# Performance work log

Hardware: AMD Instinct MI355X
Metric: run time of the kernel (lower is better)

The kernel has to match this reference:

```python
import jax, jax.numpy as jnp
import numpy as np

EPS = 1e-8
LEAK = 0.2


def upsample_linear_2x(x):
    # PyTorch nn.Upsample(scale_factor=2, mode='linear', align_corners=False) on [B,C,L]
    B, C, L = x.shape
    Lo = 2 * L
    coords = jnp.maximum((jnp.arange(Lo, dtype=jnp.float32) + 0.5) / 2.0 - 0.5, 0.0)
    i0 = jnp.minimum(jnp.floor(coords).astype(jnp.int32), L - 1)
    i1 = jnp.minimum(i0 + 1, L - 1)
    w = (coords - i0.astype(jnp.float32)).astype(x.dtype)
    return x[..., i0] * (1.0 - w) + x[..., i1] * w


def mod_conv1d(x, style, W, demod=True):
    # Style-modulated conv (StyleGAN2 Conv2DMod adapted to 1D).
    # x: [B,C,L], style: [B,C], W: [F,C,K]. Equivalent to per-sample weight
    # W*(style+1) (optionally demodulated) via input scaling + shared conv.
    s = style + 1.0
    pad = (W.shape[-1] - 1) // 2
    y = jax.lax.conv_general_dilated(x * s[:, :, None], W, (1,), [(pad, pad)],
                                     dimension_numbers=('NCH', 'OIH', 'NCH'))
    if demod:
        wmod = W[None] * s[:, None, :, None]              # [B,F,C,K]
        d = jax.lax.rsqrt(jnp.sum(wmod * wmod, axis=(2, 3)) + EPS)  # [B,F]
        y = y * d[:, :, None]
    return y


def setup_inputs() -> dict:
    key = jax.random.key(0)
    ks = jax.random.split(key, 12)
    B, Cin, F, L, Z = 8, 256, 128, 2048, 256
    Lu = 2 * L
    inp = {}
    inp['x'] = jax.random.normal(ks[0], (B, Cin, L), jnp.float32)
    inp['prev_rgb'] = jax.random.normal(ks[1], (B, 1, Lu), jnp.float32)
    inp['istyle'] = jax.random.normal(ks[2], (B, Z), jnp.float32)
    inp['inoise'] = jax.random.normal(ks[3], (B, 100), jnp.float32)
    # learned parameters
    inp['style1_w'] = jax.random.normal(ks[4], (Cin, Z), jnp.float32) * 0.02
    inp['style1_b'] = jnp.zeros((Cin,), jnp.float32)
    inp['conv1_w'] = jax.random.normal(ks[5], (F, Cin, 3), jnp.float32) * 0.05
    inp['noise_w1'] = jax.random.normal(ks[6], (F * Lu, 100), jnp.float32) * 0.01
    inp['style2_w'] = jax.random.normal(ks[7], (F, Z), jnp.float32) * 0.02
    inp['style2_b'] = jnp.zeros((F,), jnp.float32)
    inp['conv2_w'] = jax.random.normal(ks[8], (F, F, 3), jnp.float32) * 0.05
    inp['noise_w2'] = jax.random.normal(ks[9], (F * Lu, 100), jnp.float32) * 0.01
    inp['rgb_style_w'] = jax.random.normal(ks[10], (F, Z), jnp.float32) * 0.02
    inp['rgb_style_b'] = jnp.zeros((F,), jnp.float32)
    inp['rgb_conv_w'] = jax.random.normal(ks[11], (1, F, 1), jnp.float32) * 0.05
    return inp


def reference(x, prev_rgb, istyle, inoise, style1_w, style1_b, conv1_w, noise_w1,
              style2_w, style2_b, conv2_w, noise_w2, rgb_style_w, rgb_style_b, rgb_conv_w):
    x = upsample_linear_2x(x)                                 # [B,Cin,Lu]
    s1 = istyle @ style1_w.T + style1_b                       # [B,Cin]
    x = mod_conv1d(x, s1, conv1_w, demod=True)                # [B,F,Lu]
    n1 = (inoise @ noise_w1.T).reshape(x.shape)               # noise injection 1
    x = jax.nn.leaky_relu(x + n1, LEAK)
    s2 = istyle @ style2_w.T + style2_b                       # [B,F]
    x = mod_conv1d(x, s2, conv2_w, demod=True)                # [B,F,Lu]
    n2 = (inoise @ noise_w2.T).reshape(x.shape)               # noise injection 2
    x = jax.nn.leaky_relu(x + n2, LEAK)
    srgb = istyle @ rgb_style_w.T + rgb_style_b               # [B,F]
    rgb = jnp.einsum('bcl,fc->bfl', x * (srgb + 1.0)[:, :, None], rgb_conv_w[:, :, 0])
    rgb = rgb + prev_rgb
    rgb = upsample_linear_2x(rgb)                             # [B,1,2*Lu]
    return (x, rgb)
```

## Files before the change

kernel.cpp:

```cpp
#include <hip/hip_runtime.h>
#include <hip/hip_bf16.h>

#define EPS 1e-8f
#define LEAK 0.2f

#define B 8
#define CIN 256
#define F 128
#define L 2048
#define LU 4096
#define Z 256
#define NZ 100
#define S (F * LU)

typedef __attribute__((ext_vector_type(8))) short bf16x8;
typedef __attribute__((ext_vector_type(4))) float f32x4;

__device__ inline unsigned short f2bf(float x) {
    unsigned u = __builtin_bit_cast(unsigned, x);
    u += 0x7fffu + ((u >> 16) & 1u);
    return (unsigned short)(u >> 16);
}
__device__ inline float bf2f(unsigned short h) {
    unsigned u = ((unsigned)h) << 16;
    return __builtin_bit_cast(float, u);
}
__device__ inline unsigned pack2(float a, float b) {
    __hip_bfloat162 h = __float22bfloat162_rn(make_float2(a, b));
    unsigned u;
    __builtin_memcpy(&u, &h, 4);
    return u;
}
__device__ inline bf16x8 cvtfrag(float4 a, float4 b) {
    uint4 u;
    u.x = pack2(a.x, a.y); u.y = pack2(a.z, a.w);
    u.z = pack2(b.x, b.y); u.w = pack2(b.z, b.w);
    return __builtin_bit_cast(bf16x8, u);
}
__device__ inline void gload_lds16(const void* g, void* l) {
    __builtin_amdgcn_global_load_lds((const __attribute__((address_space(1))) void*)g,
                                     (__attribute__((address_space(3))) void*)l, 16, 0, 0);
}

__global__ void k_styles(const float* __restrict__ istyle,
                         const float* __restrict__ s1w, const float* __restrict__ s1b,
                         const float* __restrict__ s2w, const float* __restrict__ s2b,
                         const float* __restrict__ rgbw, const float* __restrict__ rgbb,
                         const float* __restrict__ rgbcw,
                         const float* __restrict__ W1, const float* __restrict__ W2,
                         float* __restrict__ s1, float* __restrict__ s2,
                         float* __restrict__ srgbS,
                         float* __restrict__ d1, float* __restrict__ d2,
                         unsigned short* __restrict__ Wt1, unsigned short* __restrict__ Wt2) {
    int t = threadIdx.x;
    {
        int i = blockIdx.x * 256 + t;
        if (i < 3 * F * CIN) {
            int kk = i / (F * CIN);
            int rem = i - kk * (F * CIN);
            int f = rem >> 8, c = rem & 255;
            Wt1[i] = f2bf(W1[(f * CIN + c) * 3 + kk]);
        }
        if (i < 3 * F * F) {
            int kk = i / (F * F);
            int rem = i - kk * (F * F);
            int f = rem >> 7, c = rem & 127;
            Wt2[i] = f2bf(W2[(f * F + c) * 3 + kk]);
        }
    }
    if (blockIdx.x >= 8) return;
    __shared__ float is[Z];
    __shared__ float sh1[CIN];
    __shared__ float sh2[F];
    int b = blockIdx.x;
    if (t < Z) is[t] = istyle[b * Z + t];
    __syncthreads();
    {
        float acc = 0.f;
        const float* w = s1w + (size_t)t * Z;
        for (int z = 0; z < Z; z += 4) {
            float4 v = *(const float4*)(w + z);
            acc += v.x * is[z] + v.y * is[z + 1] + v.z * is[z + 2] + v.w * is[z + 3];
        }
        float v = acc + s1b[t] + 1.0f;
        sh1[t] = v;
        s1[b * CIN + t] = v;
    }
    if (t < F) {
        float a2 = 0.f, a3 = 0.f;
        const float* w2 = s2w + (size_t)t * Z;
        const float* w3 = rgbw + (size_t)t * Z;
        for (int z = 0; z < Z; z += 4) {
            float4 u2 = *(const float4*)(w2 + z);
            float4 u3 = *(const float4*)(w3 + z);
            a2 += u2.x * is[z] + u2.y * is[z + 1] + u2.z * is[z + 2] + u2.w * is[z + 3];
            a3 += u3.x * is[z] + u3.y * is[z + 1] + u3.z * is[z + 2] + u3.w * is[z + 3];
        }
        float v2 = a2 + s2b[t] + 1.0f;
        sh2[t] = v2;
        s2[b * F + t] = v2;
        srgbS[b * F + t] = (a3 + rgbb[t] + 1.0f) * rgbcw[t];
    }
    __syncthreads();
    if (t < F) {
        float acc = 0.f;
        const float* w = W1 + (size_t)t * CIN * 3;
        for (int c = 0; c < CIN; c += 4) {
            float4 va = *(const float4*)(w + c * 3);
            float4 vb = *(const float4*)(w + c * 3 + 4);
            float4 vc = *(const float4*)(w + c * 3 + 8);
            float s0 = sh1[c], s1v = sh1[c + 1], s2v = sh1[c + 2], s3 = sh1[c + 3];
            acc += s0 * s0 * (va.x * va.x + va.y * va.y + va.z * va.z);
            acc += s1v * s1v * (va.w * va.w + vb.x * vb.x + vb.y * vb.y);
            acc += s2v * s2v * (vb.z * vb.z + vb.w * vb.w + vc.x * vc.x);
            acc += s3 * s3 * (vc.y * vc.y + vc.z * vc.z + vc.w * vc.w);
        }
        d1[b * F + t] = rsqrtf(acc + EPS);
    } else {
        int f = t - F;
        float acc = 0.f;
        const float* w = W2 + (size_t)f * F * 3;
        for (int c = 0; c < F; c += 4) {
            float4 va = *(const float4*)(w + c * 3);
            float4 vb = *(const float4*)(w + c * 3 + 4);
            float4 vc = *(const float4*)(w + c * 3 + 8);
            float s0 = sh2[c], s1v = sh2[c + 1], s2v = sh2[c + 2], s3 = sh2[c + 3];
            acc += s0 * s0 * (va.x * va.x + va.y * va.y + va.z * va.z);
            acc += s1v * s1v * (va.w * va.w + vb.x * vb.x + vb.y * vb.y);
            acc += s2v * s2v * (vb.z * vb.z + vb.w * vb.w + vc.x * vc.x);
            acc += s3 * s3 * (vc.y * vc.y + vc.z * vc.z + vc.w * vc.w);
        }
        d2[b * F + f] = rsqrtf(acc + EPS);
    }
}

__global__ __launch_bounds__(256) void k_prepx(const float* __restrict__ x,
                                               const float* __restrict__ s1,
                                               unsigned short* __restrict__ xt) {
    int b = blockIdx.z, c0 = blockIdx.y * 64, l0 = blockIdx.x * 64;
    int t = threadIdx.x;
    __shared__ float xj[64][37];
    int j0 = (l0 >> 1) - 1;
    for (int idx = t; idx < 64 * 34; idx += 256) {
        int c = idx / 34, jj = idx - c * 34;
        int j = j0 + jj;
        j = j < 0 ? 0 : (j > L - 1 ? L - 1 : j);
        xj[c][jj] = x[((size_t)(b * CIN + c0 + c)) * L + j];
    }
    __syncthreads();
    int c = t & 63;
    int lg = t >> 6;
    float s = s1[b * CIN + c0 + c];
    for (int li = 0; li < 16; ++li) {
        int ll = lg * 16 + li;
        int l = l0 + ll;
        int j = l >> 1;
        int jj = j - j0;
        float v;
        if (l & 1) {
            v = 0.75f * xj[c][jj] + 0.25f * xj[c][jj + 1];
        } else {
            v = (j == 0) ? xj[c][jj] : (0.25f * xj[c][jj - 1] + 0.75f * xj[c][jj]);
        }
        xt[((size_t)(b * LU + l)) * CIN + c0 + c] = f2bf(v * s);
    }
}

__global__ __launch_bounds__(256) void k_conv1(const unsigned short* __restrict__ xt,
                                               const unsigned short* __restrict__ Wt1,
                                               const float* __restrict__ d1,
                                               unsigned short* __restrict__ y1) {
    const int b0 = blockIdx.y * 2;
    const int l0 = blockIdx.x * 64;
    const int nfb = blockIdx.z * 4;
    const int lane = threadIdx.x & 63, wv = threadIdx.x >> 6;
    const int lbase = l0 + wv * 16;
    const int m = lane & 15, ks = lane >> 4;

    f32x4 acc[2][4];
#pragma unroll
    for (int bb = 0; bb < 2; ++bb)
#pragma unroll
        for (int nf = 0; nf < 4; ++nf) acc[bb][nf] = (f32x4)0.f;

    const unsigned short* xb0 = xt + ((size_t)(b0 + 0) * LU) * CIN + ks * 8;
    const unsigned short* xb1 = xt + ((size_t)(b0 + 1) * LU) * CIN + ks * 8;

#pragma unroll 2
    for (int kc = 0; kc < 8; ++kc) {
#pragma unroll
        for (int kk = 0; kk < 3; ++kk) {
            int lA = lbase + m + kk - 1;
            bf16x8 a0 = (bf16x8)0, a1 = (bf16x8)0;
            if (lA >= 0 && lA < LU) {
                a0 = *(const bf16x8*)&xb0[(size_t)lA * CIN + kc * 32];
                a1 = *(const bf16x8*)&xb1[(size_t)lA * CIN + kc * 32];
            }
#pragma unroll
            for (int nf = 0; nf < 4; ++nf) {
                const bf16x8 w =
                    *(const bf16x8*)&Wt1[((kk * F + (nfb + nf) * 16 + m) << 8) + kc * 32 + ks * 8];
                acc[0][nf] = __builtin_amdgcn_mfma_f32_16x16x32_bf16(a0, w, acc[0][nf], 0, 0, 0);
                acc[1][nf] = __builtin_amdgcn_mfma_f32_16x16x32_bf16(a1, w, acc[1][nf], 0, 0, 0);
            }
        }
    }
#pragma unroll
    for (int bb = 0; bb < 2; ++bb) {
        int b = b0 + bb;
#pragma unroll
        for (int nf = 0; nf < 4; ++nf) {
            int f = (nfb + nf) * 16 + m;
            float dm = d1[b * F + f];
#pragma unroll
            for (int q = 0; q < 4; ++q) {
                int l = lbase + ks * 4 + q;
                y1[((size_t)(b * LU + l) << 7) + f] = f2bf(acc[bb][nf][q] * dm);
            }
        }
    }
}

__global__ __launch_bounds__(256) void k_noise1(unsigned short* y1,
                                                const float* __restrict__ nw,
                                                const float* __restrict__ inoise,
                                                const float* __restrict__ s2) {
    __shared__ float lds[2][6400];
    const int t = threadIdx.x;
    const int lane = t & 63, wv = t >> 6;
    const int n = lane & 15, ks = lane >> 4;
    const bool w0 = (t >> 6) == 0;
    const int f0 = (blockIdx.x >> 8) * 32;
    const int l0 = (blockIdx.x & 255) * 16;
    const int r = wv * 16 + n;
    const int fseg = r >> 1, dl = r & 1;
    const int f = f0 + fseg;

    bf16x8 af[4];
#pragma unroll
    for (int ck = 0; ck < 4; ++ck) {
        bf16x8 a = (bf16x8)0;
        if (n < 8) {
            const float* ap = inoise + n * NZ;
#pragma unroll
            for (int j = 0; j < 8; ++j) {
                int z = ck * 32 + ks * 8 + j;
                if (z < NZ) a[j] = (short)f2bf(ap[z]);
            }
        }
        af[ck] = a;
    }

    unsigned short yv[8][4] = {};
    float s2v[4] = {};
    if (ks < 2) {
#pragma unroll
        for (int q = 0; q < 4; ++q) s2v[q] = s2[(ks * 4 + q) * F + f];
#pragma unroll
        for (int cc = 0; cc < 8; ++cc) {
            int l = l0 + 2 * cc + dl;
            size_t i = (size_t)l * F + f;
#pragma unroll
            for (int q = 0; q < 4; ++q) yv[cc][q] = y1[(size_t)(ks * 4 + q) * S + i];
        }
    }

    auto stage = [&](int buf, int cc) {
        const int lbase = l0 + 2 * cc;
#pragma unroll
        for (int rr = 0; rr < 7; ++rr) {
            int g = rr * 256 + t;
            if (g < 1600) {
                int fs = g / 50;
                int rem = g - fs * 50;
                int d2 = (rem >= 25) ? 1 : 0;
                int m = rem - 25 * d2;
                const float* src = nw + ((size_t)(f0 + fs) * LU + lbase + d2) * NZ + m * 4;
                gload_lds16(src, &lds[buf][g * 4]);
            }
        }
    };

    auto compute = [&](int buf, int cc) {
        const float* rowp = &lds[buf][r * 100];
        f32x4 acc = (f32x4)0.f;
#pragma unroll
        for (int ck = 0; ck < 3; ++ck) {
            float4 u0 = *(const float4*)&rowp[ck * 32 + ks * 8];
            float4 u1 = *(const float4*)&rowp[ck * 32 + ks * 8 + 4];
            acc = __builtin_amdgcn_mfma_f32_16x16x32_bf16(af[ck], cvtfrag(u0, u1), acc, 0, 0, 0);
        }
        {
            bf16x8 b3 = (bf16x8)0;
            if (ks == 0) {
                float4 u = *(const float4*)&rowp[96];
                unsigned p0 = pack2(u.x, u.y), p1 = pack2(u.z, u.w);
                b3[0] = (short)(p0 & 0xffff); b3[1] = (short)(p0 >> 16);
                b3[2] = (short)(p1 & 0xffff); b3[3] = (short)(p1 >> 16);
            }
            acc = __builtin_amdgcn_mfma_f32_16x16x32_bf16(af[3], b3, acc, 0, 0, 0);
        }
        if (ks < 2) {
            const int l = l0 + 2 * cc + dl;
            const size_t i = (size_t)l * F + f;
#pragma unroll
            for (int q = 0; q < 4; ++q) {
                float val = bf2f(yv[cc][q]) + acc[q];
                val = val >= 0.f ? val : LEAK * val;
                y1[(size_t)(ks * 4 + q) * S + i] = f2bf(val * s2v[q]);
            }
        }
    };

    stage(0, 0);
    stage(1, 1);

#define WSTEP(N0, N1)                                                       \
    if (w0) { asm volatile("s_waitcnt vmcnt(" #N0 ")" ::: "memory"); }      \
    else    { asm volatile("s_waitcnt vmcnt(" #N1 ")" ::: "memory"); }      \
    __builtin_amdgcn_s_barrier();                                           \
    __builtin_amdgcn_sched_barrier(0);

    WSTEP(7, 6)              compute(0, 0);
    WSTEP(4, 4) stage(0, 2); compute(1, 1);
    WSTEP(4, 4) stage(1, 3); compute(0, 2);
    WSTEP(4, 4) stage(0, 4); compute(1, 3);
    WSTEP(4, 4) stage(1, 5); compute(0, 4);
    WSTEP(4, 4) stage(0, 6); compute(1, 5);
    WSTEP(4, 4) stage(1, 7); compute(0, 6);
    WSTEP(4, 4)              compute(1, 7);
#undef WSTEP
}

__global__ __launch_bounds__(256) void k_conv2(const unsigned short* __restrict__ y1n,
                                               const unsigned short* __restrict__ Wt2,
                                               const float* __restrict__ d2,
                                               float* __restrict__ xout) {
    const int b0 = blockIdx.y * 2;
    const int l0 = blockIdx.x * 64;
    const int mfb = blockIdx.z * 4;
    const int lane = threadIdx.x & 63, wv = threadIdx.x >> 6;
    const int lbase = l0 + wv * 16;
    const int m = lane & 15, ks = lane >> 4;

    f32x4 acc[2][4];
#pragma unroll
    for (int bb = 0; bb < 2; ++bb)
#pragma unroll
        for (int mf = 0; mf < 4; ++mf) acc[bb][mf] = (f32x4)0.f;

    const unsigned short* yb0 = y1n + ((size_t)(b0 + 0) * LU) * F + ks * 8;
    const unsigned short* yb1 = y1n + ((size_t)(b0 + 1) * LU) * F + ks * 8;

#pragma unroll 2
    for (int kc = 0; kc < 4; ++kc) {
#pragma unroll
        for (int kk = 0; kk < 3; ++kk) {
            int lB = lbase + m + kk - 1;
            bf16x8 bv0 = (bf16x8)0, bv1 = (bf16x8)0;
            if (lB >= 0 && lB < LU) {
                bv0 = *(const bf16x8*)&yb0[(size_t)lB * F + kc * 32];
                bv1 = *(const bf16x8*)&yb1[(size_t)lB * F + kc * 32];
            }
#pragma unroll
            for (int mf = 0; mf < 4; ++mf) {
                const bf16x8 w =
                    *(const bf16x8*)&Wt2[((kk * F + (mfb + mf) * 16 + m) << 7) + kc * 32 + ks * 8];
                acc[0][mf] = __builtin_amdgcn_mfma_f32_16x16x32_bf16(w, bv0, acc[0][mf], 0, 0, 0);
                acc[1][mf] = __builtin_amdgcn_mfma_f32_16x16x32_bf16(w, bv1, acc[1][mf], 0, 0, 0);
            }
        }
    }
#pragma unroll
    for (int bb = 0; bb < 2; ++bb) {
        int b = b0 + bb;
#pragma unroll
        for (int mf = 0; mf < 4; ++mf) {
#pragma unroll
            for (int q = 0; q < 4; ++q) {
                int f = (mfb + mf) * 16 + ks * 4 + q;
                int l = lbase + m;
                xout[((size_t)(b * F + f) << 12) + l] = acc[bb][mf][q] * d2[b * F + f];
            }
        }
    }
}

__global__ __launch_bounds__(256) void k_noise2(const float* __restrict__ nw,
                                                const float* __restrict__ inoise,
                                                float* xio) {
    __shared__ float lds[2][6400];
    const int t = threadIdx.x;
    const int lane = t & 63, wv = t >> 6;
    const int n = lane & 15, ks = lane >> 4;
    const bool w0 = (t >> 6) == 0;
    const int row0 = blockIdx.x * 512;
    const int r = wv * 16 + n;

    bf16x8 af[4];
#pragma unroll
    for (int ck = 0; ck < 4; ++ck) {
        bf16x8 a = (bf16x8)0;
        if (n < 8) {
            const float* ap = inoise + n * NZ;
#pragma unroll
            for (int j = 0; j < 8; ++j) {
                int z = ck * 32 + ks * 8 + j;
                if (z < NZ) a[j] = (short)f2bf(ap[z]);
            }
        }
        af[ck] = a;
    }

    float xv[8][4] = {};
    if (ks < 2) {
#pragma unroll
        for (int cc = 0; cc < 8; ++cc) {
            size_t i = (size_t)row0 + cc * 64 + r;
#pragma unroll
            for (int q = 0; q < 4; ++q) xv[cc][q] = xio[(size_t)(ks * 4 + q) * S + i];
        }
    }

    auto stage = [&](int buf, int cc) {
        const float* src0 = nw + ((size_t)row0 + cc * 64) * NZ;
#pragma unroll
        for (int rr = 0; rr < 7; ++rr) {
            int g = rr * 256 + t;
            if (g < 1600) gload_lds16(src0 + g * 4, &lds[buf][g * 4]);
        }
    };

    auto compute = [&](int buf, int cc) {
        const float* rowp = &lds[buf][r * 100];
        f32x4 acc = (f32x4)0.f;
#pragma unroll
        for (int ck = 0; ck < 3; ++ck) {
            float4 u0 = *(const float4*)&rowp[ck * 32 + ks * 8];
            float4 u1 = *(const float4*)&rowp[ck * 32 + ks * 8 + 4];
            acc = __builtin_amdgcn_mfma_f32_16x16x32_bf16(af[ck], cvtfrag(u0, u1), acc, 0, 0, 0);
        }
        {
            bf16x8 b3 = (bf16x8)0;
            if (ks == 0) {
                float4 u = *(const float4*)&rowp[96];
                unsigned p0 = pack2(u.x, u.y), p1 = pack2(u.z, u.w);
                b3[0] = (short)(p0 & 0xffff); b3[1] = (short)(p0 >> 16);
                b3[2] = (short)(p1 & 0xffff); b3[3] = (short)(p1 >> 16);
            }
            acc = __builtin_amdgcn_mfma_f32_16x16x32_bf16(af[3], b3, acc, 0, 0, 0);
        }
        if (ks < 2) {
            const size_t i = (size_t)row0 + cc * 64 + r;
#pragma unroll
            for (int q = 0; q < 4; ++q) {
                float val = xv[cc][q] + acc[q];
                val = val >= 0.f ? val : LEAK * val;
                xio[(size_t)(ks * 4 + q) * S + i] = val;
            }
        }
    };

    stage(0, 0);
    stage(1, 1);

#define WSTEP(N0, N1)                                                       \
    if (w0) { asm volatile("s_waitcnt vmcnt(" #N0 ")" ::: "memory"); }      \
    else    { asm volatile("s_waitcnt vmcnt(" #N1 ")" ::: "memory"); }      \
    __builtin_amdgcn_s_barrier();                                           \
    __builtin_amdgcn_sched_barrier(0);

    WSTEP(7, 6)              compute(0, 0);
    WSTEP(4, 4) stage(0, 2); compute(1, 1);
    WSTEP(4, 4) stage(1, 3); compute(0, 2);
    WSTEP(4, 4) stage(0, 4); compute(1, 3);
    WSTEP(4, 4) stage(1, 5); compute(0, 4);
    WSTEP(4, 4) stage(0, 6); compute(1, 5);
    WSTEP(4, 4) stage(1, 7); compute(0, 6);
    WSTEP(4, 4)              compute(1, 7);
#undef WSTEP
}

__global__ __launch_bounds__(256) void k_rgb(const float* __restrict__ xf,
                                             const float* __restrict__ srgbS,
                                             const float* __restrict__ prev,
                                             float* __restrict__ rgb) {
    int b = blockIdx.y;
    int o0 = blockIdx.x * 512;
    int t = threadIdx.x;
    __shared__ float ss[F];
    __shared__ float pre[258];
    if (t < F) ss[t] = srgbS[b * F + t];
    __syncthreads();
    int j0 = (o0 >> 1) - 1;
    for (int jj = t; jj < 258; jj += 256) {
        int j = j0 + jj;
        j = j < 0 ? 0 : (j > LU - 1 ? LU - 1 : j);
        float acc = prev[b * LU + j];
        const float* xb = xf + (size_t)b * S + j;
        for (int f = 0; f < F; ++f) acc += xb[(size_t)f * LU] * ss[f];
        pre[jj] = acc;
    }
    __syncthreads();
    int jj = t + 1;
    int j = j0 + jj;
    float ve = (j == 0) ? pre[jj] : (0.25f * pre[jj - 1] + 0.75f * pre[jj]);
    float vo = 0.75f * pre[jj] + 0.25f * pre[jj + 1];
    float2 v2 = make_float2(ve, vo);
    *(float2*)&rgb[(size_t)b * 2 * LU + o0 + 2 * t] = v2;
}

extern "C" void kernel_launch(void* const* d_in, const int* in_sizes, int n_in,
                              void* d_out, int out_size, void* d_ws, size_t ws_size,
                              hipStream_t stream) {
    const float* x      = (const float*)d_in[0];
    const float* prev   = (const float*)d_in[1];
    const float* istyle = (const float*)d_in[2];
    const float* inoise = (const float*)d_in[3];
    const float* s1w    = (const float*)d_in[4];
    const float* s1b    = (const float*)d_in[5];
    const float* W1     = (const float*)d_in[6];
    const float* nw1    = (const float*)d_in[7];
    const float* s2w    = (const float*)d_in[8];
    const float* s2b    = (const float*)d_in[9];
    const float* W2     = (const float*)d_in[10];
    const float* nw2    = (const float*)d_in[11];
    const float* rgbw   = (const float*)d_in[12];
    const float* rgbb   = (const float*)d_in[13];
    const float* rgbcw  = (const float*)d_in[14];

    char* w = (char*)d_ws;
    float* s1      = (float*)(w);
    float* s2      = (float*)(w + 8 * 1024);
    float* srgbS   = (float*)(w + 12 * 1024);
    float* d1      = (float*)(w + 16 * 1024);
    float* d2      = (float*)(w + 20 * 1024);
    unsigned short* Wt1 = (unsigned short*)(w + 256 * 1024);
    unsigned short* Wt2 = (unsigned short*)(w + 448 * 1024);
    unsigned short* y1  = (unsigned short*)(w + (size_t)1024 * 1024);

    unsigned short* xt = (unsigned short*)d_out;

    float* xout   = (float*)d_out;
    float* rgbout = xout + (size_t)B * S;

    k_styles<<<384, 256, 0, stream>>>(istyle, s1w, s1b, s2w, s2b, rgbw, rgbb, rgbcw,
                                      W1, W2, s1, s2, srgbS, d1, d2, Wt1, Wt2);
    k_prepx<<<dim3(LU / 64, CIN / 64, B), 256, 0, stream>>>(x, s1, xt);
    k_conv1<<<dim3(LU / 64, B / 2, 2), 256, 0, stream>>>(xt, Wt1, d1, y1);
    k_noise1<<<1024, 256, 0, stream>>>(y1, nw1, inoise, s2);
    k_conv2<<<dim3(LU / 64, B / 2, 2), 256, 0, stream>>>(y1, Wt2, d2, xout);
    k_noise2<<<1024, 256, 0, stream>>>(nw2, inoise, xout);
    k_rgb<<<dim3(2 * LU / 512, B), 256, 0, stream>>>(xout, srgbS, prev, rgbout);
}
```

Measured before the change: 239.5 us.

## Merge conv1 and both noise GEMMs into one launch, apply noise later

Conv1 and the two noise-projection GEMMs now run together in one grid, split by block index, so the memory-bound noise-weight streaming can overlap with the conv1 MFMA work. The noise results go to new bf16 scratch buffers. A small elementwise kernel then adds noise 1, applies leaky-relu and the s2 scale. Noise 2 and its leaky-relu are folded into the conv2 epilogue, which removes the separate read-modify-write pass over the fp32 output. In exchange it writes and reads two extra bf16 intermediates, adds one launch, and rounds noise 2 to bf16 before adding it.

```diff
diff --git a/kernel.cpp b/kernel.cpp
--- a/kernel.cpp
+++ b/kernel.cpp
@@ -166,75 +166,81 @@
     }
 }
 
-__global__ __launch_bounds__(256) void k_conv1(const unsigned short* __restrict__ xt,
-                                               const unsigned short* __restrict__ Wt1,
-                                               const float* __restrict__ d1,
-                                               unsigned short* __restrict__ y1) {
-    const int b0 = blockIdx.y * 2;
-    const int l0 = blockIdx.x * 64;
-    const int nfb = blockIdx.z * 4;
-    const int lane = threadIdx.x & 63, wv = threadIdx.x >> 6;
-    const int lbase = l0 + wv * 16;
-    const int m = lane & 15, ks = lane >> 4;
-
-    f32x4 acc[2][4];
-#pragma unroll
-    for (int bb = 0; bb < 2; ++bb)
-#pragma unroll
-        for (int nf = 0; nf < 4; ++nf) acc[bb][nf] = (f32x4)0.f;
-
-    const unsigned short* xb0 = xt + ((size_t)(b0 + 0) * LU) * CIN + ks * 8;
-    const unsigned short* xb1 = xt + ((size_t)(b0 + 1) * LU) * CIN + ks * 8;
-
-#pragma unroll 2
-    for (int kc = 0; kc < 8; ++kc) {
-#pragma unroll
-        for (int kk = 0; kk < 3; ++kk) {
-            int lA = lbase + m + kk - 1;
-            bf16x8 a0 = (bf16x8)0, a1 = (bf16x8)0;
-            if (lA >= 0 && lA < LU) {
-                a0 = *(const bf16x8*)&xb0[(size_t)lA * CIN + kc * 32];
-                a1 = *(const bf16x8*)&xb1[(size_t)lA * CIN + kc * 32];
-            }
-#pragma unroll
-            for (int nf = 0; nf < 4; ++nf) {
-                const bf16x8 w =
-                    *(const bf16x8*)&Wt1[((kk * F + (nfb + nf) * 16 + m) << 8) + kc * 32 + ks * 8];
-                acc[0][nf] = __builtin_amdgcn_mfma_f32_16x16x32_bf16(a0, w, acc[0][nf], 0, 0, 0);
-                acc[1][nf] = __builtin_amdgcn_mfma_f32_16x16x32_bf16(a1, w, acc[1][nf], 0, 0, 0);
-            }
-        }
-    }
-#pragma unroll
-    for (int bb = 0; bb < 2; ++bb) {
-        int b = b0 + bb;
-#pragma unroll
-        for (int nf = 0; nf < 4; ++nf) {
-            int f = (nfb + nf) * 16 + m;
-            float dm = d1[b * F + f];
-#pragma unroll
-            for (int q = 0; q < 4; ++q) {
-                int l = lbase + ks * 4 + q;
-                y1[((size_t)(b * LU + l) << 7) + f] = f2bf(acc[bb][nf][q] * dm);
-            }
-        }
-    }
-}
-
-__global__ __launch_bounds__(256) void k_noise1(unsigned short* y1,
-                                                const float* __restrict__ nw,
-                                                const float* __restrict__ inoise,
-                                                const float* __restrict__ s2) {
+#define WSTEP(N0, N1)                                                       \
+    if (w0) { asm volatile("s_waitcnt vmcnt(" #N0 ")" ::: "memory"); }      \
+    else    { asm volatile("s_waitcnt vmcnt(" #N1 ")" ::: "memory"); }      \
+    __builtin_amdgcn_s_barrier();                                           \
+    __builtin_amdgcn_sched_barrier(0);
+
+__global__ __launch_bounds__(256) void k_mega(const unsigned short* __restrict__ xt,
+                                              const unsigned short* __restrict__ Wt1,
+                                              const float* __restrict__ d1,
+                                              unsigned short* __restrict__ y1,
+                                              const float* __restrict__ nw1,
+                                              const float* __restrict__ nw2,
+                                              const float* __restrict__ inoise,
+                                              unsigned short* __restrict__ n1buf,
+                                              unsigned short* __restrict__ n2buf) {
     __shared__ float lds[2][6400];
+    const int bid = blockIdx.x;
     const int t = threadIdx.x;
     const int lane = t & 63, wv = t >> 6;
+
+    if (bid < 512) {
+        const int b0 = ((bid >> 6) & 3) * 2;
+        const int l0 = (bid & 63) * 64;
+        const int nfb = (bid >> 8) * 4;
+        const int lbase = l0 + wv * 16;
+        const int m = lane & 15, ks = lane >> 4;
+
+        f32x4 acc[2][4];
+#pragma unroll
+        for (int bb = 0; bb < 2; ++bb)
+#pragma unroll
+            for (int nf = 0; nf < 4; ++nf) acc[bb][nf] = (f32x4)0.f;
+
+        const unsigned short* xb0 = xt + ((size_t)(b0 + 0) * LU) * CIN + ks * 8;
+        const unsigned short* xb1 = xt + ((size_t)(b0 + 1) * LU) * CIN + ks * 8;
+
+#pragma unroll 2
+        for (int kc = 0; kc < 8; ++kc) {
+#pragma unroll
+            for (int kk = 0; kk < 3; ++kk) {
+                int lA = lbase + m + kk - 1;
+                bf16x8 a0 = (bf16x8)0, a1 = (bf16x8)0;
+                if (lA >= 0 && lA < LU) {
+                    a0 = *(const bf16x8*)&xb0[(size_t)lA * CIN + kc * 32];
+                    a1 = *(const bf16x8*)&xb1[(size_t)lA * CIN + kc * 32];
+                }
+#pragma unroll
+                for (int nf = 0; nf < 4; ++nf) {
+                    const bf16x8 w =
+                        *(const bf16x8*)&Wt1[((kk * F + (nfb + nf) * 16 + m) << 8) + kc * 32 + ks * 8];
+                    acc[0][nf] = __builtin_amdgcn_mfma_f32_16x16x32_bf16(a0, w, acc[0][nf], 0, 0, 0);
+                    acc[1][nf] = __builtin_amdgcn_mfma_f32_16x16x32_bf16(a1, w, acc[1][nf], 0, 0, 0);
+                }
+            }
+        }
+#pragma unroll
+        for (int bb = 0; bb < 2; ++bb) {
+            int b = b0 + bb;
+#pragma unroll
+            for (int nf = 0; nf < 4; ++nf) {
+                int f = (nfb + nf) * 16 + m;
+                float dm = d1[b * F + f];
+#pragma unroll
+                for (int q = 0; q < 4; ++q) {
+                    int l = lbase + ks * 4 + q;
+                    y1[((size_t)(b * LU + l) << 7) + f] = f2bf(acc[bb][nf][q] * dm);
+                }
+            }
+        }
+        return;
+    }
+
     const int n = lane & 15, ks = lane >> 4;
     const bool w0 = (t >> 6) == 0;
-    const int f0 = (blockIdx.x >> 8) * 32;
-    const int l0 = (blockIdx.x & 255) * 16;
     const int r = wv * 16 + n;
-    const int fseg = r >> 1, dl = r & 1;
-    const int f = f0 + fseg;
 
     bf16x8 af[4];
 #pragma unroll
@@ -251,37 +257,81 @@
         af[ck] = a;
     }
 
-    unsigned short yv[8][4] = {};
-    float s2v[4] = {};
-    if (ks < 2) {
-#pragma unroll
-        for (int q = 0; q < 4; ++q) s2v[q] = s2[(ks * 4 + q) * F + f];
-#pragma unroll
-        for (int cc = 0; cc < 8; ++cc) {
-            int l = l0 + 2 * cc + dl;
-            size_t i = (size_t)l * F + f;
-#pragma unroll
-            for (int q = 0; q < 4; ++q) yv[cc][q] = y1[(size_t)(ks * 4 + q) * S + i];
-        }
-    }
-
-    auto stage = [&](int buf, int cc) {
-        const int lbase = l0 + 2 * cc;
+    if (bid < 1536) {
+        const int bid2 = bid - 512;
+        const int f0 = (bid2 >> 8) * 32;
+        const int l0 = (bid2 & 255) * 16;
+        const int fseg = r >> 1, dl = r & 1;
+        const int f = f0 + fseg;
+
+        auto stage = [&](int buf, int cc) {
+            const int lbase = l0 + 2 * cc;
+#pragma unroll
+            for (int rr = 0; rr < 7; ++rr) {
+                int g = rr * 256 + t;
+                if (g < 1600) {
+                    int fs = g / 50;
+                    int rem = g - fs * 50;
+                    int d2v = (rem >= 25) ? 1 : 0;
+                    int m = rem - 25 * d2v;
+                    const float* src = nw1 + ((size_t)(f0 + fs) * LU + lbase + d2v) * NZ + m * 4;
+                    gload_lds16(src, &lds[buf][g * 4]);
+                }
+            }
+        };
+        auto compute = [&](int buf, int cc) {
+            const float* rowp = &lds[buf][r * 100];
+            f32x4 acc = (f32x4)0.f;
+#pragma unroll
+            for (int ck = 0; ck < 3; ++ck) {
+                float4 u0 = *(const float4*)&rowp[ck * 32 + ks * 8];
+                float4 u1 = *(const float4*)&rowp[ck * 32 + ks * 8 + 4];
+                acc = __builtin_amdgcn_mfma_f32_16x16x32_bf16(af[ck], cvtfrag(u0, u1), acc, 0, 0, 0);
+            }
+            {
+                bf16x8 b3 = (bf16x8)0;
+                if (ks == 0) {
+                    float4 u = *(const float4*)&rowp[96];
+                    unsigned p0 = pack2(u.x, u.y), p1 = pack2(u.z, u.w);
+                    b3[0] = (short)(p0 & 0xffff); b3[1] = (short)(p0 >> 16);
+                    b3[2] = (short)(p1 & 0xffff); b3[3] = (short)(p1 >> 16);
+                }
+                acc = __builtin_amdgcn_mfma_f32_16x16x32_bf16(af[3], b3, acc, 0, 0, 0);
+            }
+            if (ks < 2) {
+                const int l = l0 + 2 * cc + dl;
+                const size_t i = (size_t)l * F + f;
+#pragma unroll
+                for (int q = 0; q < 4; ++q)
+                    n1buf[(size_t)(ks * 4 + q) * S + i] = f2bf(acc[q]);
+            }
+        };
+
+        stage(0, 0);
+        stage(1, 1);
+        WSTEP(7, 6)              compute(0, 0);
+        WSTEP(4, 4) stage(0, 2); compute(1, 1);
+        WSTEP(4, 4) stage(1, 3); compute(0, 2);
+        WSTEP(4, 4) stage(0, 4); compute(1, 3);
+        WSTEP(4, 4) stage(1, 5); compute(0, 4);
+        WSTEP(4, 4) stage(0, 6); compute(1, 5);
+        WSTEP(4, 4) stage(1, 7); compute(0, 6);
+        WSTEP(4, 4)              compute(1, 7);
+        return;
+    }
+
+    const int bid3 = bid - 1536;
+    const int row0 = bid3 * 512;
+
+    auto stage2 = [&](int buf, int cc) {
+        const float* src0 = nw2 + ((size_t)row0 + cc * 64) * NZ;
 #pragma unroll
         for (int rr = 0; rr < 7; ++rr) {
             int g = rr * 256 + t;
-            if (g < 1600) {
-                int fs = g / 50;
-                int rem = g - fs * 50;
-                int d2 = (rem >= 25) ? 1 : 0;
-                int m = rem - 25 * d2;
-                const float* src = nw + ((size_t)(f0 + fs) * LU + lbase + d2) * NZ + m * 4;
-                gload_lds16(src, &lds[buf][g * 4]);
-            }
+            if (g < 1600) gload_lds16(src0 + g * 4, &lds[buf][g * 4]);
         }
     };
-
-    auto compute = [&](int buf, int cc) {
+    auto compute2 = [&](int buf, int cc) {
         const float* rowp = &lds[buf][r * 100];
         f32x4 acc = (f32x4)0.f;
 #pragma unroll
@@ -301,40 +351,48 @@
             acc = __builtin_amdgcn_mfma_f32_16x16x32_bf16(af[3], b3, acc, 0, 0, 0);
         }
         if (ks < 2) {
-            const int l = l0 + 2 * cc + dl;
-            const size_t i = (size_t)l * F + f;
-#pragma unroll
-            for (int q = 0; q < 4; ++q) {
-                float val = bf2f(yv[cc][q]) + acc[q];
-                val = val >= 0.f ? val : LEAK * val;
-                y1[(size_t)(ks * 4 + q) * S + i] = f2bf(val * s2v[q]);
-            }
+            const size_t i = (size_t)row0 + cc * 64 + r;
+#pragma unroll
+            for (int q = 0; q < 4; ++q)
+                n2buf[(size_t)(ks * 4 + q) * S + i] = f2bf(acc[q]);
         }
     };
 
-    stage(0, 0);
-    stage(1, 1);
-
-#define WSTEP(N0, N1)                                                       \
-    if (w0) { asm volatile("s_waitcnt vmcnt(" #N0 ")" ::: "memory"); }      \
-    else    { asm volatile("s_waitcnt vmcnt(" #N1 ")" ::: "memory"); }      \
-    __builtin_amdgcn_s_barrier();                                           \
-    __builtin_amdgcn_sched_barrier(0);
-
-    WSTEP(7, 6)              compute(0, 0);
-    WSTEP(4, 4) stage(0, 2); compute(1, 1);
-    WSTEP(4, 4) stage(1, 3); compute(0, 2);
-    WSTEP(4, 4) stage(0, 4); compute(1, 3);
-    WSTEP(4, 4) stage(1, 5); compute(0, 4);
-    WSTEP(4, 4) stage(0, 6); compute(1, 5);
-    WSTEP(4, 4) stage(1, 7); compute(0, 6);
-    WSTEP(4, 4)              compute(1, 7);
+    stage2(0, 0);
+    stage2(1, 1);
+    WSTEP(7, 6)               compute2(0, 0);
+    WSTEP(4, 4) stage2(0, 2); compute2(1, 1);
+    WSTEP(4, 4) stage2(1, 3); compute2(0, 2);
+    WSTEP(4, 4) stage2(0, 4); compute2(1, 3);
+    WSTEP(4, 4) stage2(1, 5); compute2(0, 4);
+    WSTEP(4, 4) stage2(0, 6); compute2(1, 5);
+    WSTEP(4, 4) stage2(1, 7); compute2(0, 6);
+    WSTEP(4, 4)               compute2(1, 7);
+}
 #undef WSTEP
+
+__global__ __launch_bounds__(256) void k_apply1(unsigned short* y1,
+                                                const unsigned short* __restrict__ n1,
+                                                const float* __restrict__ s2) {
+    __shared__ float s2s[B][F];
+    int t = threadIdx.x;
+    for (int idx = t; idx < B * F; idx += 256) s2s[idx >> 7][idx & 127] = s2[idx];
+    __syncthreads();
+    int i = blockIdx.x * 256 + t;
+    int f = i & 127;
+#pragma unroll
+    for (int bb = 0; bb < B; ++bb) {
+        size_t a = (size_t)bb * S + i;
+        float v = bf2f(y1[a]) + bf2f(n1[a]);
+        v = v >= 0.f ? v : LEAK * v;
+        y1[a] = f2bf(v * s2s[bb][f]);
+    }
 }
 
 __global__ __launch_bounds__(256) void k_conv2(const unsigned short* __restrict__ y1n,
                                                const unsigned short* __restrict__ Wt2,
                                                const float* __restrict__ d2,
+                                               const unsigned short* __restrict__ n2buf,
                                                float* __restrict__ xout) {
     const int b0 = blockIdx.y * 2;
     const int l0 = blockIdx.x * 64;
@@ -380,105 +438,13 @@
             for (int q = 0; q < 4; ++q) {
                 int f = (mfb + mf) * 16 + ks * 4 + q;
                 int l = lbase + m;
-                xout[((size_t)(b * F + f) << 12) + l] = acc[bb][mf][q] * d2[b * F + f];
-            }
-        }
-    }
-}
-
-__global__ __launch_bounds__(256) void k_noise2(const float* __restrict__ nw,
-                                                const float* __restrict__ inoise,
-                                                float* xio) {
-    __shared__ float lds[2][6400];
-    const int t = threadIdx.x;
-    const int lane = t & 63, wv = t >> 6;
-    const int n = lane & 15, ks = lane >> 4;
-    const bool w0 = (t >> 6) == 0;
-    const int row0 = blockIdx.x * 512;
-    const int r = wv * 16 + n;
-
-    bf16x8 af[4];
-#pragma unroll
-    for (int ck = 0; ck < 4; ++ck) {
-        bf16x8 a = (bf16x8)0;
-        if (n < 8) {
-            const float* ap = inoise + n * NZ;
-#pragma unroll
-            for (int j = 0; j < 8; ++j) {
-                int z = ck * 32 + ks * 8 + j;
-                if (z < NZ) a[j] = (short)f2bf(ap[z]);
-            }
-        }
-        af[ck] = a;
-    }
-
-    float xv[8][4] = {};
-    if (ks < 2) {
-#pragma unroll
-        for (int cc = 0; cc < 8; ++cc) {
-            size_t i = (size_t)row0 + cc * 64 + r;
-#pragma unroll
-            for (int q = 0; q < 4; ++q) xv[cc][q] = xio[(size_t)(ks * 4 + q) * S + i];
-        }
-    }
-
-    auto stage = [&](int buf, int cc) {
-        const float* src0 = nw + ((size_t)row0 + cc * 64) * NZ;
-#pragma unroll
-        for (int rr = 0; rr < 7; ++rr) {
-            int g = rr * 256 + t;
-            if (g < 1600) gload_lds16(src0 + g * 4, &lds[buf][g * 4]);
-        }
-    };
-
-    auto compute = [&](int buf, int cc) {
-        const float* rowp = &lds[buf][r * 100];
-        f32x4 acc = (f32x4)0.f;
-#pragma unroll
-        for (int ck = 0; ck < 3; ++ck) {
-            float4 u0 = *(const float4*)&rowp[ck * 32 + ks * 8];
-            float4 u1 = *(const float4*)&rowp[ck * 32 + ks * 8 + 4];
-            acc = __builtin_amdgcn_mfma_f32_16x16x32_bf16(af[ck], cvtfrag(u0, u1), acc, 0, 0, 0);
-        }
-        {
-            bf16x8 b3 = (bf16x8)0;
-            if (ks == 0) {
-                float4 u = *(const float4*)&rowp[96];
-                unsigned p0 = pack2(u.x, u.y), p1 = pack2(u.z, u.w);
-                b3[0] = (short)(p0 & 0xffff); b3[1] = (short)(p0 >> 16);
-                b3[2] = (short)(p1 & 0xffff); b3[3] = (short)(p1 >> 16);
-            }
-            acc = __builtin_amdgcn_mfma_f32_16x16x32_bf16(af[3], b3, acc, 0, 0, 0);
-        }
-        if (ks < 2) {
-            const size_t i = (size_t)row0 + cc * 64 + r;
-#pragma unroll
-            for (int q = 0; q < 4; ++q) {
-                float val = xv[cc][q] + acc[q];
+                size_t i = ((size_t)f << 12) + l;
+                float val = acc[bb][mf][q] * d2[b * F + f] + bf2f(n2buf[(size_t)b * S + i]);
                 val = val >= 0.f ? val : LEAK * val;
-                xio[(size_t)(ks * 4 + q) * S + i] = val;
-            }
-        }
-    };
-
-    stage(0, 0);
-    stage(1, 1);
-
-#define WSTEP(N0, N1)                                                       \
-    if (w0) { asm volatile("s_waitcnt vmcnt(" #N0 ")" ::: "memory"); }      \
-    else    { asm volatile("s_waitcnt vmcnt(" #N1 ")" ::: "memory"); }      \
-    __builtin_amdgcn_s_barrier();                                           \
-    __builtin_amdgcn_sched_barrier(0);
-
-    WSTEP(7, 6)              compute(0, 0);
-    WSTEP(4, 4) stage(0, 2); compute(1, 1);
-    WSTEP(4, 4) stage(1, 3); compute(0, 2);
-    WSTEP(4, 4) stage(0, 4); compute(1, 3);
-    WSTEP(4, 4) stage(1, 5); compute(0, 4);
-    WSTEP(4, 4) stage(0, 6); compute(1, 5);
-    WSTEP(4, 4) stage(1, 7); compute(0, 6);
-    WSTEP(4, 4)              compute(1, 7);
-#undef WSTEP
+                xout[(size_t)b * S + i] = val;
+            }
+        }
+    }
 }
 
 __global__ __launch_bounds__(256) void k_rgb(const float* __restrict__ xf,
@@ -537,7 +503,9 @@
     float* d2      = (float*)(w + 20 * 1024);
     unsigned short* Wt1 = (unsigned short*)(w + 256 * 1024);
     unsigned short* Wt2 = (unsigned short*)(w + 448 * 1024);
-    unsigned short* y1  = (unsigned short*)(w + (size_t)1024 * 1024);
+    unsigned short* y1    = (unsigned short*)(w + (size_t)1 * 1024 * 1024);
+    unsigned short* n1buf = (unsigned short*)(w + (size_t)10 * 1024 * 1024);
+    unsigned short* n2buf = (unsigned short*)(w + (size_t)19 * 1024 * 1024);
 
     unsigned short* xt = (unsigned short*)d_out;
 
@@ -547,9 +515,8 @@
     k_styles<<<384, 256, 0, stream>>>(istyle, s1w, s1b, s2w, s2b, rgbw, rgbb, rgbcw,
                                       W1, W2, s1, s2, srgbS, d1, d2, Wt1, Wt2);
     k_prepx<<<dim3(LU / 64, CIN / 64, B), 256, 0, stream>>>(x, s1, xt);
-    k_conv1<<<dim3(LU / 64, B / 2, 2), 256, 0, stream>>>(xt, Wt1, d1, y1);
-    k_noise1<<<1024, 256, 0, stream>>>(y1, nw1, inoise, s2);
-    k_conv2<<<dim3(LU / 64, B / 2, 2), 256, 0, stream>>>(y1, Wt2, d2, xout);
-    k_noise2<<<1024, 256, 0, stream>>>(nw2, inoise, xout);
+    k_mega<<<2560, 256, 0, stream>>>(xt, Wt1, d1, y1, nw1, nw2, inoise, n1buf, n2buf);
+    k_apply1<<<S / 256, 256, 0, stream>>>(y1, n1buf, s2);
+    k_conv2<<<dim3(LU / 64, B / 2, 2), 256, 0, stream>>>(y1, Wt2, d2, n2buf, xout);
     k_rgb<<<dim3(2 * LU / 512, B), 256, 0, stream>>>(xout, srgbS, prev, rgbout);
 }
```

After: 224.9 us. 1.07x faster.
